# Kernel tuning notes

Measured on AMD Instinct MI355X. Metric: run time of the kernel, lower is better.

## Reference

```python
import jax, jax.numpy as jnp
import numpy as np

B, S, D, H = 4, 2048, 1024, 16  # batch, seq, n_embd, n_head
HD = D // H  # head size = 64


def setup_inputs() -> dict:
    key = jax.random.key(0)
    ks = jax.random.split(key, 5)
    s = 0.02
    return {
        "x": jax.random.normal(ks[0], (B, S, D), dtype=jnp.float32),
        "W_attn": jax.random.normal(ks[1], (D, 3 * D), dtype=jnp.float32) * s,
        "b_attn": jnp.zeros((3 * D,), dtype=jnp.float32),
        "W_proj": jax.random.normal(ks[2], (D, D), dtype=jnp.float32) * s,
        "b_proj": jnp.zeros((D,), dtype=jnp.float32),
    }


def reference(x, W_attn, b_attn, W_proj, b_proj):
    Bx, Sx, Dx = x.shape
    qkv = x @ W_attn + b_attn  # [B,S,3D]
    q, k, v = jnp.split(qkv, 3, axis=-1)
    # [B,H,S,hd]
    q = q.reshape(Bx, Sx, H, HD).transpose(0, 2, 1, 3)
    k = k.reshape(Bx, Sx, H, HD).transpose(0, 2, 1, 3)
    v = v.reshape(Bx, Sx, H, HD).transpose(0, 2, 1, 3)
    scale = 1.0 / jnp.sqrt(jnp.asarray(HD, dtype=x.dtype))
    att = jnp.einsum("bhqd,bhkd->bhqk", q, k) * scale  # [B,H,S,S]
    causal = jnp.tril(jnp.ones((Sx, Sx), dtype=bool))
    att = jnp.where(causal[None, None, :, :], att, jnp.asarray(-jnp.inf, dtype=att.dtype))
    att = jax.nn.softmax(att, axis=-1)
    y = jnp.einsum("bhqk,bhkd->bhqd", att, v)  # [B,H,S,hd]
    y = y.transpose(0, 2, 1, 3).reshape(Bx, Sx, Dx)
    return y @ W_proj + b_proj
```

## Files before the change

### kernel.cpp

```cpp
#include <hip/hip_runtime.h>
#include <math.h>

#define SEQ 2048
#define DIM 1024
#define NH 16
#define HD 64
#define QKV_LD 3072

typedef __attribute__((ext_vector_type(8))) __bf16 bf16x8;
typedef __attribute__((ext_vector_type(8))) unsigned short u16x8;
typedef __attribute__((ext_vector_type(4))) unsigned short u16x4;
typedef __attribute__((ext_vector_type(4))) float f32x4;

typedef unsigned int __attribute__((may_alias)) u32a;

__device__ __forceinline__ unsigned short f2b(float f) {
  unsigned int b = __builtin_bit_cast(unsigned int, f);
  return (unsigned short)((b + 0x7fffu + ((b >> 16) & 1u)) >> 16);
}

__device__ __forceinline__ void gload_lds16(const void* g, void* l) {
  __builtin_amdgcn_global_load_lds((const __attribute__((address_space(1))) void*)g,
                                   (__attribute__((address_space(3))) void*)l,
                                   16, 0, 0);
}

__device__ __forceinline__ bf16x8 ld_frag16(const unsigned short* p) {
  bf16x8 r;
  __builtin_memcpy(&r, __builtin_assume_aligned((void*)p, 16), 16);
  return r;
}

#define BARRIER_VM4()  asm volatile("s_waitcnt vmcnt(4)\ns_barrier" ::: "memory")
#define BARRIER_LGKM() asm volatile("s_waitcnt lgkmcnt(0)\ns_barrier" ::: "memory")
#define ISSUE_FENCE()  asm volatile("" ::: "memory")


__global__ void to_bf16_kernel(const float* __restrict__ x,
                               unsigned short* __restrict__ y, int n) {
  int i = (blockIdx.x * blockDim.x + threadIdx.x) * 4;
  if (i >= n) return;
  float4 v = *(const float4*)(x + i);
  u16x4 o;
  o.x = f2b(v.x); o.y = f2b(v.y); o.z = f2b(v.z); o.w = f2b(v.w);
  *(u16x4*)(y + i) = o;
}

__global__ void transpose_to_bf16_kernel(const float* __restrict__ W,
                                         unsigned short* __restrict__ WT,
                                         int K, int N) {
  __shared__ float tile[32][33];
  const int n0 = blockIdx.x * 32, k0 = blockIdx.y * 32;
  const int tx = threadIdx.x, ty = threadIdx.y;
  tile[ty][tx] = W[(size_t)(k0 + ty) * N + n0 + tx];
  __syncthreads();
  WT[(size_t)(n0 + ty) * K + k0 + tx] = f2b(tile[tx][ty]);
}


template <int OUT_F32>
__global__ __launch_bounds__(256, 2) void gemm_bt_kernel(
    const unsigned short* __restrict__ A,
    const unsigned short* __restrict__ BT,
    const float* __restrict__ bias,
    void* __restrict__ C, int M, int N, int K,
    int scale_cols, float scale_val) {
  __shared__ unsigned short As[128 * 32];
  __shared__ unsigned short Bs[128 * 32];

  const int tid = threadIdx.x;
  const int wave = tid >> 6;
  const int lane = tid & 63;
  const int quad = lane >> 4;
  const int l16 = lane & 15;
  const int m0 = blockIdx.y * 128;
  const int n0 = blockIdx.x * 128;
  const int wm = (wave >> 1) * 64;
  const int wn = (wave & 1) * 64;

  const size_t a_g = (size_t)(m0 + wave * 32 + (lane >> 2)) * K + (lane & 3) * 8;
  const size_t b_g = (size_t)(n0 + wave * 32 + (lane >> 2)) * K + (lane & 3) * 8;
  unsigned short* lA = As + wave * 1024;
  unsigned short* lB = Bs + wave * 1024;

  f32x4 acc[4][4] = {};

  for (int k0 = 0; k0 < K; k0 += 32) {
    gload_lds16(A + a_g + k0, lA);
    gload_lds16(A + a_g + (size_t)16 * K + k0, lA + 512);
    gload_lds16(BT + b_g + k0, lB);
    gload_lds16(BT + b_g + (size_t)16 * K + k0, lB + 512);
    __syncthreads();

    bf16x8 af[4], bfr[4];
#pragma unroll
    for (int i = 0; i < 4; ++i)
      af[i] = *(const bf16x8*)&As[(wm + i * 16 + l16) * 32 + quad * 8];
#pragma unroll
    for (int i = 0; i < 4; ++i)
      bfr[i] = *(const bf16x8*)&Bs[(wn + i * 16 + l16) * 32 + quad * 8];
#pragma unroll
    for (int mi = 0; mi < 4; ++mi)
#pragma unroll
      for (int ni = 0; ni < 4; ++ni)
        acc[mi][ni] = __builtin_amdgcn_mfma_f32_16x16x32_bf16(af[mi], bfr[ni],
                                                              acc[mi][ni], 0, 0, 0);
    __syncthreads();
  }

#pragma unroll
  for (int mi = 0; mi < 4; ++mi) {
#pragma unroll
    for (int ni = 0; ni < 4; ++ni) {
      const int col = n0 + wn + ni * 16 + l16;
      const int row = m0 + wm + mi * 16 + quad * 4;
      const float bv = bias[col];
      const float sv = (col < scale_cols) ? scale_val : 1.0f;
#pragma unroll
      for (int r = 0; r < 4; ++r) {
        float v = (acc[mi][ni][r] + bv) * sv;
        if (OUT_F32)
          ((float*)C)[(size_t)(row + r) * N + col] = v;
        else
          ((unsigned short*)C)[(size_t)(row + r) * N + col] = f2b(v);
      }
    }
  }
}


#define FA_PREFETCH(g_, via_, vib_)                                            \
  {                                                                            \
    const int _g = (g_);                                                       \
    const int _tg = (_g < kt) ? _g : 0;                                        \
    const unsigned short* _kg =                                                \
        base + (size_t)(_tg * 64 + ktok_l) * QKV_LD + DIM + h * HD + kchunk * 8; \
    gload_lds16(_kg, &Ks[_g % 3][0][w * 512]);                                 \
    gload_lds16(_kg + 32, &Ks[_g % 3][1][w * 512]);                            \
    const unsigned short* _vg =                                                \
        base + (size_t)(_tg * 64 + 2 * vk) * QKV_LD + 2 * DIM + h * HD + vc;   \
    via_ = *(const u16x8*)_vg;                                                 \
    vib_ = *(const u16x8*)(_vg + QKV_LD);                                      \
  }

#define VT_WRITE(va_, vb_)                                                     \
  {                                                                            \
    u32a* _V32 = (u32a*)Vt;                                                    \
    _Pragma("unroll") for (int j = 0; j < 8; ++j)                              \
      _V32[vwidx[j]] = (unsigned int)(va_)[j] | ((unsigned int)(vb_)[j] << 16);\
  }

#define FA_COMPUTE(i_, t_, kt_, qf_)                                           \
  {                                                                            \
    const unsigned short* _kb0 = &Ks[(i_) % 3][0][0];                          \
    const unsigned short* _kb1 = &Ks[(i_) % 3][1][0];                          \
    bf16x8 kf0[4], kf1[4], vf0[4], vf1[4];                                     \
    _Pragma("unroll") for (int ni = 0; ni < 4; ++ni) {                         \
      const int ro = (ni * 16 + l16) * 32 + ((quad ^ rsw) * 8);                \
      kf0[ni] = ld_frag16(_kb0 + ro);                                          \
      kf1[ni] = ld_frag16(_kb1 + ro);                                          \
      vf0[ni] = ld_frag16(&Vt[quad * 512 + vroff[ni]]);                        \
      vf1[ni] = ld_frag16(&Vt[(4 + quad) * 512 + vroff[ni]]);                  \
    }                                                                          \
    const int qloc = w * 16 + quad * 4;                                        \
    _Pragma("unroll") for (int m = 0; m < 2; ++m) {                            \
      if (!(m == 0 && (t_) == (kt_)-1)) {   \
        const bool diag = ((t_) == (kt_)-2 + m);                               \
        _Pragma("unroll") for (int ni = 0; ni < 4; ++ni) {                     \
          f32x4 a = {};                                                        \
          a = __builtin_amdgcn_mfma_f32_16x16x32_bf16(qf_[m][0], kf0[ni], a, 0, 0, 0); \
          a = __builtin_amdgcn_mfma_f32_16x16x32_bf16(qf_[m][1], kf1[ni], a, 0, 0, 0); \
          const int kloc = ni * 16 + l16;                                      \
          _Pragma("unroll") for (int r = 0; r < 4; ++r) {                      \
            float p = __builtin_amdgcn_exp2f(a[r]);                            \
            if (diag && kloc > qloc + r) p = 0.0f;                 \
            Ps[w][(quad * 4 + r) * 72 + kloc] =                                \
                (unsigned short)(__builtin_bit_cast(unsigned int, p) >> 16);   \
          }                                                                    \
        }                                                                      \
        _Pragma("unroll") for (int c = 0; c < 2; ++c) {                        \
          const bf16x8 pa = ld_frag16(&Ps[w][l16 * 72 + c * 32 + quad * 8]);   \
          _Pragma("unroll") for (int ni = 0; ni < 4; ++ni)                     \
            o[m][ni] = __builtin_amdgcn_mfma_f32_16x16x32_bf16(                \
                pa, c ? vf1[ni] : vf0[ni], o[m][ni], 0, 0, 0);                 \
          lacc[m] = __builtin_amdgcn_mfma_f32_16x16x32_bf16(pa, onesb,         \
                                                            lacc[m], 0, 0, 0);\
        }                                                                      \
      }                                                                        \
    }                                                                          \
  }

#define FA_ITER(i_, t_, kt_, qf_, pva, pvb, cva, cvb)                          \
  {                                                                            \
    FA_PREFETCH((i_) + 2, pva, pvb);                                           \
    FA_COMPUTE(i_, t_, kt_, qf_);                                              \
    BARRIER_VM4();                                                             \
    if ((i_) + 1 < (kt_)) {                                                    \
      VT_WRITE(cva, cvb);                                                      \
      BARRIER_LGKM();                                                          \
    }                                                                          \
  }

#define FA_EPILOGUE(q0_)                                                       \
  _Pragma("unroll") for (int m = 0; m < 2; ++m)                                \
  _Pragma("unroll") for (int r = 0; r < 4; ++r) {                              \
    const float lv = __shfl(lacc[m][r], quad << 4);                            \
    const float inv = 1.0f / lv;                                               \
    const int row = (q0_) + m * 64 + w * 16 + quad * 4 + r;                    \
    unsigned short* dst = yatt + (size_t)(b * SEQ + row) * DIM + h * HD + l16; \
    _Pragma("unroll") for (int ni = 0; ni < 4; ++ni)                           \
      dst[ni * 16] = f2b(o[m][ni][r] * inv);                                   \
  }

__global__ __launch_bounds__(256, 2) void flash_kernel(
    const unsigned short* __restrict__ qkv,
    unsigned short* __restrict__ yatt) {
  __shared__ unsigned short Ks[3][2][64 * 32];
  __shared__ __align__(16) unsigned short Vt[8 * 64 * 8];
  __shared__ __align__(16) unsigned short Ps[4][16 * 72];

  const int tid = threadIdx.x;
  const int w = tid >> 6;
  const int lane = tid & 63;
  const int quad = lane >> 4;
  const int l16 = lane & 15;

  const int bid = (int)blockIdx.x;
  const int qt = 15 - (bid >> 6);
  const int bh = bid & 63;
  const int b = bh >> 4;
  const int h = bh & 15;
  const int kt = 2 * qt + 2;
  const int q0 = qt * 128;

  const unsigned short* base = qkv + (size_t)b * SEQ * QKV_LD;

  const int ktok_l = w * 16 + (lane >> 2);
  const int ksw = (ktok_l ^ (ktok_l >> 2)) & 3;
  const int kchunk = (lane & 3) ^ ksw;
  const int rsw = (l16 ^ (l16 >> 2)) & 3;

  const int vk = tid >> 3;
  const int vc = (tid & 7) * 8;
  int vwidx[8];
#pragma unroll
  for (int j = 0; j < 8; ++j)
    vwidx[j] = (vk >> 2) * 256 + (vc | ((j + (vc >> 3)) & 7)) * 4 + (vk & 3);
  int vroff[4];
#pragma unroll
  for (int ni = 0; ni < 4; ++ni) {
    const int dim = ni * 16 + l16;
    vroff[ni] = ((dim & 56) | ((dim + (dim >> 3)) & 7)) * 8;
  }

  u16x8 ob = {};
  if (l16 == 0) {
#pragma unroll
    for (int j = 0; j < 8; ++j) ob[j] = 0x3F80;
  }
  const bf16x8 onesb = __builtin_bit_cast(bf16x8, ob);

  bf16x8 qf[2][2];
#pragma unroll
  for (int m = 0; m < 2; ++m) {
    const unsigned short* qa =
        base + (size_t)(q0 + m * 64 + w * 16 + l16) * QKV_LD + h * HD + quad * 8;
    qf[m][0] = *(const bf16x8*)qa;
    qf[m][1] = *(const bf16x8*)(qa + 32);
  }

  u16x8 va0, vb0, va1, vb1;
  ISSUE_FENCE();
  FA_PREFETCH(0, va0, vb0);
  ISSUE_FENCE();
  FA_PREFETCH(1, va1, vb1);
  BARRIER_VM4();
  VT_WRITE(va0, vb0);
  BARRIER_LGKM();

  f32x4 o[2][4] = {};
  f32x4 lacc[2] = {};

  for (int i = 0; i < kt; i += 2) {
    FA_ITER(i,     i,     kt, qf, va0, vb0, va1, vb1);
    FA_ITER(i + 1, i + 1, kt, qf, va1, vb1, va0, vb0);
  }
  FA_EPILOGUE(q0);
}


extern "C" void kernel_launch(void* const* d_in, const int* in_sizes, int n_in,
                              void* d_out, int out_size, void* d_ws, size_t ws_size,
                              hipStream_t stream) {
  const float* x  = (const float*)d_in[0];
  const float* Wa = (const float*)d_in[1];
  const float* ba = (const float*)d_in[2];
  const float* Wp = (const float*)d_in[3];
  const float* bp = (const float*)d_in[4];
  float* out = (float*)d_out;

  char* ws = (char*)d_ws;
  unsigned short* xb   = (unsigned short*)ws;
  unsigned short* WaT  = (unsigned short*)(ws + 16777216);
  unsigned short* WpT  = (unsigned short*)(ws + 23068672);
  unsigned short* qkv  = (unsigned short*)(ws + 25165824);
  unsigned short* yatt = (unsigned short*)(ws + 75497472);

  const int M = 4 * SEQ;
  const float qscale = 0.125f * 1.44269504089f;

  to_bf16_kernel<<<8192, 256, 0, stream>>>(x, xb, M * DIM);
  transpose_to_bf16_kernel<<<dim3(96, 32), dim3(32, 32), 0, stream>>>(Wa, WaT, DIM, 3 * DIM);
  transpose_to_bf16_kernel<<<dim3(32, 32), dim3(32, 32), 0, stream>>>(Wp, WpT, DIM, DIM);

  gemm_bt_kernel<0><<<dim3(24, 64), 256, 0, stream>>>(xb, WaT, ba, qkv, M, 3 * DIM, DIM,
                                                      DIM, qscale);

  flash_kernel<<<dim3(1024), 256, 0, stream>>>(qkv, yatt);

  gemm_bt_kernel<1><<<dim3(8, 64), 256, 0, stream>>>(yatt, WpT, bp, out, M, DIM, DIM,
                                                     0, 1.0f);
}
```

Measured before the change: 261.3 us.

## Triple-buffer GEMM LDS stages with XOR-swizzled layout to overlap loads

The bf16 GEMM mainloop now uses a three-stage LDS ring: it prefetches tile t+2 while computing tile t, and each iteration ends with a single barrier that waits on outstanding vector-memory counts. The global-to-LDS load columns are XOR-swizzled by row, with a matching read offset, to reduce LDS bank conflicts on fragment reads. This targets global-load latency stalls and the double barrier per k-step, at the cost of three times the LDS use, which may lower occupancy. The last tiles re-prefetch tile NT-1 into the ring as redundant loads.

New measurement: 262.8 us. No clear change (+0.6%).

```diff
diff --git a/kernel.cpp b/kernel.cpp
--- a/kernel.cpp
+++ b/kernel.cpp
@@ -65,8 +65,8 @@
     const float* __restrict__ bias,
     void* __restrict__ C, int M, int N, int K,
     int scale_cols, float scale_val) {
-  __shared__ unsigned short As[128 * 32];
-  __shared__ unsigned short Bs[128 * 32];
+  __shared__ __align__(16) unsigned short As[3][128 * 32];
+  __shared__ __align__(16) unsigned short Bs[3][128 * 32];
 
   const int tid = threadIdx.x;
   const int wave = tid >> 6;
@@ -78,34 +78,53 @@
   const int wm = (wave >> 1) * 64;
   const int wn = (wave & 1) * 64;
 
-  const size_t a_g = (size_t)(m0 + wave * 32 + (lane >> 2)) * K + (lane & 3) * 8;
-  const size_t b_g = (size_t)(n0 + wave * 32 + (lane >> 2)) * K + (lane & 3) * 8;
-  unsigned short* lA = As + wave * 1024;
-  unsigned short* lB = Bs + wave * 1024;
+  const int srow = lane >> 2;
+  const int scol8 = (lane & 3) ^ (srow & 3);
+  const size_t a_g0 = (size_t)(m0 + wave * 32 + srow) * K + scol8 * 8;
+  const size_t a_g1 = a_g0 + (size_t)16 * K;
+  const size_t b_g0 = (size_t)(n0 + wave * 32 + srow) * K + scol8 * 8;
+  const size_t b_g1 = b_g0 + (size_t)16 * K;
+  const int lds_o0 = wave * 1024;
+  const int lds_o1 = wave * 1024 + 512;
+
+  const int rdc = (quad ^ (l16 & 3)) * 8;
 
   f32x4 acc[4][4] = {};
-
-  for (int k0 = 0; k0 < K; k0 += 32) {
-    gload_lds16(A + a_g + k0, lA);
-    gload_lds16(A + a_g + (size_t)16 * K + k0, lA + 512);
-    gload_lds16(BT + b_g + k0, lB);
-    gload_lds16(BT + b_g + (size_t)16 * K + k0, lB + 512);
-    __syncthreads();
-
-    bf16x8 af[4], bfr[4];
+  const int NT = K >> 5;
+
+#define G_STAGE(kt_, buf_)                                                     \
+  {                                                                            \
+    const int _k0 = (kt_) << 5;                                                \
+    gload_lds16(A + a_g0 + _k0, &As[buf_][lds_o0]);                            \
+    gload_lds16(A + a_g1 + _k0, &As[buf_][lds_o1]);                            \
+    gload_lds16(BT + b_g0 + _k0, &Bs[buf_][lds_o0]);                           \
+    gload_lds16(BT + b_g1 + _k0, &Bs[buf_][lds_o1]);                           \
+  }
+
+  G_STAGE(0, 0);
+  ISSUE_FENCE();
+  G_STAGE(1, 1);
+  BARRIER_VM4();
+
+  for (int t = 0; t < NT; ++t) {
+    const int pf = (t + 2 < NT) ? t + 2 : NT - 1;
+    G_STAGE(pf, (t + 2) % 3);
+
+    const unsigned short* la = As[t % 3];
+    const unsigned short* lb = Bs[t % 3];
+    bf16x8 af[4];
 #pragma unroll
     for (int i = 0; i < 4; ++i)
-      af[i] = *(const bf16x8*)&As[(wm + i * 16 + l16) * 32 + quad * 8];
-#pragma unroll
-    for (int i = 0; i < 4; ++i)
-      bfr[i] = *(const bf16x8*)&Bs[(wn + i * 16 + l16) * 32 + quad * 8];
-#pragma unroll
-    for (int mi = 0; mi < 4; ++mi)
-#pragma unroll
-      for (int ni = 0; ni < 4; ++ni)
-        acc[mi][ni] = __builtin_amdgcn_mfma_f32_16x16x32_bf16(af[mi], bfr[ni],
+      af[i] = ld_frag16(&la[(wm + i * 16 + l16) * 32 + rdc]);
+#pragma unroll
+    for (int ni = 0; ni < 4; ++ni) {
+      const bf16x8 bf = ld_frag16(&lb[(wn + ni * 16 + l16) * 32 + rdc]);
+#pragma unroll
+      for (int mi = 0; mi < 4; ++mi)
+        acc[mi][ni] = __builtin_amdgcn_mfma_f32_16x16x32_bf16(af[mi], bf,
                                                               acc[mi][ni], 0, 0, 0);
-    __syncthreads();
+    }
+    BARRIER_VM4();
   }
 
 #pragma unroll
```
